# Kernel optimization log

Measured on AMD Instinct MI355X. Metric: run time of the kernel, lower is better.

## Reference

```python
import jax, jax.numpy as jnp
import numpy as np

NLT_SIZES = (10, 19, 39, 69, 12)  # agent, action, duplex, triplet, loc
ALPHA, GAMMA, BETA = 0.25, 2.0, 1.0 / 9.0
B, A, G, T = 8, 60000, 20, 5
C = 1 + sum(NLT_SIZES)  # 150


def setup_inputs() -> dict:
    key = jax.random.key(0)
    ks = jax.random.split(key, 8)
    confidence = jax.random.normal(ks[0], (B, A, C), jnp.float32)
    predicted_locations = jax.random.normal(ks[1], (B, A, 4), jnp.float32)
    gt_locations = jax.random.normal(ks[2], (B, A, 4), jnp.float32)
    counts = jax.random.randint(ks[3], (B,), 1, G + 1, dtype=jnp.int32)
    # gt_labels: [B, G, nlts, T] with -1 tail padding per (gt, label-type) row
    labs = []
    for i, nc in enumerate(NLT_SIZES):
        l = jax.random.randint(jax.random.fold_in(ks[4], i), (B, G, T), 0, nc, dtype=jnp.int32)
        nvalid = jax.random.randint(jax.random.fold_in(ks[5], i), (B, G, 1), 1, T + 1, dtype=jnp.int32)
        l = jnp.where(jnp.arange(T, dtype=jnp.int32)[None, None, :] < nvalid, l, -1)
        labs.append(l)
    gt_labels = jnp.stack(labs, axis=2)  # [B, G, 5, T]
    # labels_bin: per-anchor match result: -1 ignore, 0 background, k in [1, counts[b]] matched gt
    pos_idx = jax.random.randint(ks[6], (B, A), 1, G + 1, dtype=jnp.int32)
    pos_idx = jnp.minimum(pos_idx, counts[:, None])
    u = jax.random.uniform(ks[7], (B, A))
    labels_bin = jnp.where(u < 0.90, 0, jnp.where(u < 0.95, -1, pos_idx)).astype(jnp.int32)
    return {
        "confidence": confidence,
        "predicted_locations": predicted_locations,
        "gt_locations": gt_locations,
        "gt_labels": gt_labels,
        "counts": counts,
        "labels_bin": labels_bin,
    }


def _head_labels(gt_labels_nlt, labels_bin, numc):
    # gt_labels_nlt: [B, G, T] int, -1 tail-padded. Vectorized one_hot_labels + gather.
    valid = (gt_labels_nlt >= 0)
    oh = jax.nn.one_hot(jnp.where(valid, gt_labels_nlt, 0), numc, dtype=jnp.float32)
    oh = oh * valid[..., None].astype(jnp.float32)
    table = (oh.sum(axis=2) > 0).astype(jnp.float32)  # [B, G, numc], multi-hot per gt
    table = jnp.pad(table, ((0, 0), (1, 0), (0, 0)))  # row 0 = background zeros -> [B, G+1, numc]
    idx = jnp.clip(labels_bin, 0, None)  # dumy_conf: ignores (-1) map to row 0
    return jnp.take_along_axis(table, idx[:, :, None], axis=1)  # [B, A, numc]


def _focal(preds, labels, mask, num_pos):
    p = jnp.clip(preds, 1e-7, 1.0 - 1e-7)
    bce = -(labels * jnp.log(p) + (1.0 - labels) * jnp.log1p(-p))
    alpha_factor = ALPHA * labels + (1.0 - ALPHA) * (1.0 - labels)
    pt = p * labels + (1.0 - p) * (1.0 - labels)
    return (bce * alpha_factor * (1.0 - pt) ** GAMMA * mask).sum() / num_pos


def reference(confidence, predicted_locations, gt_locations, gt_labels, counts, labels_bin):
    sig = jax.nn.sigmoid(confidence)
    binary_preds = sig[:, :, 0]
    heads = []
    cc = 1
    for nc in NLT_SIZES:
        heads.append(sig[:, :, cc:cc + nc])
        cc += nc

    pos = (labels_bin > 0).astype(jnp.float32)  # pos_mask
    num_pos = jnp.maximum(1.0, pos.sum())

    n = jnp.abs(predicted_locations - gt_locations)
    sl1 = jnp.where(n < BETA, 0.5 * n * n / BETA, n - 0.5 * BETA)
    regression_loss = (sl1 * pos[:, :, None]).sum() / (num_pos * 4.0)

    mask = (labels_bin > -1).astype(jnp.float32)  # exclude ignored anchors
    cls_loss = 0.0
    for i, nc in enumerate(NLT_SIZES):
        labs = _head_labels(gt_labels[:, :, i, :], labels_bin, nc)
        cls_loss = cls_loss + _focal(heads[i], labs, mask[:, :, None], num_pos)
    cls_loss = cls_loss + _focal(binary_preds, pos, mask, num_pos)  # binary head: labels_bin>0 -> 1
    return (regression_loss, cls_loss / 6.0)
```

## Files before the change

### kernel.cpp

```cpp
#include <hip/hip_runtime.h>

#define B_    8
#define A_    60000
#define C_    150
#define G_    20
#define T_    5
#define ROWS  21
#define NANCH (B_ * A_)
#define NTOT  (B_ * A_ * C_)
#define TABN  (B_ * ROWS * C_)
#define BETA_ (1.0f / 9.0f)

__global__ void build_table(const int* __restrict__ gt_labels,
                            float* __restrict__ tab,
                            float* __restrict__ accum) {
    int i = blockIdx.x * blockDim.x + threadIdx.x;
    if (i < 4) accum[i] = 0.0f;
    if (i >= TABN) return;
    int c  = i % C_;
    int bg = i / C_;
    int g  = bg % ROWS;
    int b  = bg / ROWS;
    float v = 0.0f;
    if (g > 0) {
        if (c == 0) {
            v = 1.0f;
        } else {
            int cc = c - 1;
            int head, k;
            if      (cc < 10)  { head = 0; k = cc; }
            else if (cc < 29)  { head = 1; k = cc - 10; }
            else if (cc < 68)  { head = 2; k = cc - 29; }
            else if (cc < 137) { head = 3; k = cc - 68; }
            else               { head = 4; k = cc - 137; }
            const int* lp = gt_labels + ((b * G_ + (g - 1)) * 5 + head) * T_;
            v = (lp[0] == k || lp[1] == k || lp[2] == k ||
                 lp[3] == k || lp[4] == k) ? 1.0f : 0.0f;
        }
    }
    tab[i] = v;
}

__device__ __forceinline__ float block_reduce_sum(float v, float* sm) {
    #pragma unroll
    for (int off = 32; off > 0; off >>= 1) v += __shfl_down(v, off, 64);
    int lane = threadIdx.x & 63, w = threadIdx.x >> 6;
    if (lane == 0) sm[w] = v;
    __syncthreads();
    float r = 0.0f;
    if (threadIdx.x == 0) r = sm[0] + sm[1] + sm[2] + sm[3];
    __syncthreads();
    return r;
}

__device__ __forceinline__ float sl1(float n) {
    return (n < BETA_) ? (0.5f / BETA_) * n * n : n - 0.5f * BETA_;
}

__global__ __launch_bounds__(256) void reg_kernel(
        const float* __restrict__ pred, const float* __restrict__ gt,
        const int* __restrict__ lb, float* __restrict__ accum) {
    __shared__ float sm[4];
    float reg = 0.0f, cnt = 0.0f;
    int stride = gridDim.x * blockDim.x;
    for (int a = blockIdx.x * blockDim.x + threadIdx.x; a < NANCH; a += stride) {
        int l = lb[a];
        if (l > 0) {
            cnt += 1.0f;
            float4 p = ((const float4*)pred)[a];
            float4 g = ((const float4*)gt)[a];
            reg += sl1(fabsf(p.x - g.x)) + sl1(fabsf(p.y - g.y)) +
                   sl1(fabsf(p.z - g.z)) + sl1(fabsf(p.w - g.w));
        }
    }
    float rblk = block_reduce_sum(reg, sm);
    float cblk = block_reduce_sum(cnt, sm);
    if (threadIdx.x == 0) {
        atomicAdd(&accum[0], rblk);
        atomicAdd(&accum[2], cblk);
    }
}

__global__ __launch_bounds__(256) void cls_kernel(
        const float* __restrict__ conf, const int* __restrict__ lb,
        const float* __restrict__ tab, float* __restrict__ accum) {
    __shared__ float sm[4];
    float acc = 0.0f;
    const float4* cp = (const float4*)conf;
    const int nchunks = NTOT / 4;
    int stride = gridDim.x * blockDim.x;
    for (int ch = blockIdx.x * blockDim.x + threadIdx.x; ch < nchunks; ch += stride) {
        int e = ch * 4;
        float4 x = cp[ch];
        int a  = e / C_;
        int c  = e - a * C_;
        int l0 = lb[a];
        bool spans = (c + 3 >= C_);
        int l1 = spans ? lb[a + 1] : l0;

        if ((l0 | l1) == 0) {
            float xs[4] = {x.x, x.y, x.z, x.w};
            #pragma unroll
            for (int j = 0; j < 4; ++j) {
                float t = __expf(xs[j]);
                float denom = 1.0f + t;
                float om = t * __builtin_amdgcn_rcpf(denom);
                acc += 0.75f * (om * om) * __logf(denom);
            }
        } else if (l0 == -1 && l1 == -1) {
        } else {
            int b0 = a / A_;
            int row0 = (b0 * ROWS + max(l0, 0)) * C_;
            float m0 = (l0 > -1) ? 1.0f : 0.0f;
            int row1 = row0; float m1 = m0;
            if (spans) {
                int b1 = (a + 1) / A_;
                row1 = (b1 * ROWS + max(l1, 0)) * C_;
                m1 = (l1 > -1) ? 1.0f : 0.0f;
            }
            float xs[4] = {x.x, x.y, x.z, x.w};
            #pragma unroll
            for (int j = 0; j < 4; ++j) {
                int cj = c + j;
                int rb; float mf;
                if (cj < C_) { rb = row0 + cj;      mf = m0; }
                else         { rb = row1 + cj - C_; mf = m1; }
                float L = tab[rb];
                float s = (L + L - 1.0f) * xs[j];
                float t = __expf(-s);
                float denom = 1.0f + t;
                float om  = t * __builtin_amdgcn_rcpf(denom);
                float ld  = __logf(denom);
                acc += mf * fmaf(L, -0.5f, 0.75f) * (om * om) * ld;
            }
        }
    }
    float blk = block_reduce_sum(acc, sm);
    if (threadIdx.x == 0) atomicAdd(&accum[1], blk);
}

__global__ void finalize(const float* __restrict__ accum, float* __restrict__ out) {
    float np = fmaxf(1.0f, accum[2]);
    out[0] = accum[0] / (np * 4.0f);
    out[1] = accum[1] / (np * 6.0f);
}

extern "C" void kernel_launch(void* const* d_in, const int* in_sizes, int n_in,
                              void* d_out, int out_size, void* d_ws, size_t ws_size,
                              hipStream_t stream) {
    const float* conf = (const float*)d_in[0];
    const float* pred = (const float*)d_in[1];
    const float* gt   = (const float*)d_in[2];
    const int*   gtl  = (const int*)d_in[3];
    const int*   lb   = (const int*)d_in[5];
    float* out   = (float*)d_out;
    float* accum = (float*)d_ws;
    float* tab   = (float*)d_ws + 64;

    build_table<<<(TABN + 255) / 256, 256, 0, stream>>>(gtl, tab, accum);
    reg_kernel<<<512, 256, 0, stream>>>(pred, gt, lb, accum);
    cls_kernel<<<4096, 256, 0, stream>>>(conf, lb, tab, accum);
    finalize<<<1, 1, 0, stream>>>(accum, out);
}
```

Before: 442.3 us.

## Fuse regression and classification kernels, unroll loads, use deterministic partial reduction

Merges the regression and classification passes into one grid-stride kernel over 8192 blocks. The classification loop is unrolled two-wide so two float4 loads are in flight per thread. The fast background path now uses a wave-uniform __any test, which avoids divergence. Atomics are replaced by per-block partials that a 256-thread finalize kernel reduces. Fully ignored chunks no longer get an early exit and are computed with a zero mask, which adds some transcendental work.

```diff
diff --git a/kernel.cpp b/kernel.cpp
--- a/kernel.cpp
+++ b/kernel.cpp
@@ -1,21 +1,22 @@
 #include <hip/hip_runtime.h>
 
-#define B_    8
-#define A_    60000
-#define C_    150
-#define G_    20
-#define T_    5
-#define ROWS  21
-#define NANCH (B_ * A_)
-#define NTOT  (B_ * A_ * C_)
-#define TABN  (B_ * ROWS * C_)
-#define BETA_ (1.0f / 9.0f)
+#define B_     8
+#define A_     60000
+#define C_     150
+#define G_     20
+#define T_     5
+#define ROWS   21
+#define NANCH  (B_ * A_)
+#define NTOT   (B_ * A_ * C_)
+#define NCHUNK (NTOT / 4)
+#define TABN   (B_ * ROWS * C_)
+#define BETA_  (1.0f / 9.0f)
+#define NBLK   8192
+#define TPB    256
 
 __global__ void build_table(const int* __restrict__ gt_labels,
-                            float* __restrict__ tab,
-                            float* __restrict__ accum) {
+                            float* __restrict__ tab) {
     int i = blockIdx.x * blockDim.x + threadIdx.x;
-    if (i < 4) accum[i] = 0.0f;
     if (i >= TABN) return;
     int c  = i % C_;
     int bg = i / C_;
@@ -57,92 +58,120 @@
     return (n < BETA_) ? (0.5f / BETA_) * n * n : n - 0.5f * BETA_;
 }
 
-__global__ __launch_bounds__(256) void reg_kernel(
-        const float* __restrict__ pred, const float* __restrict__ gt,
-        const int* __restrict__ lb, float* __restrict__ accum) {
+__device__ __forceinline__ float focal_term(float x, float L, float mf) {
+    float s     = (L + L - 1.0f) * x;
+    float t     = __expf(-s);
+    float denom = 1.0f + t;
+    float om    = t * __builtin_amdgcn_rcpf(denom);
+    float ld    = __logf(denom);
+    return mf * fmaf(L, -0.5f, 0.75f) * (om * om) * ld;
+}
+
+__device__ __forceinline__ float process_chunk(float4 x, int a, int c,
+                                               int l0, int l1,
+                                               const float* __restrict__ tab) {
+    float acc = 0.0f;
+    float xs[4] = {x.x, x.y, x.z, x.w};
+    if (!__any((l0 | l1) != 0)) {
+        #pragma unroll
+        for (int j = 0; j < 4; ++j) {
+            float t     = __expf(xs[j]);
+            float denom = 1.0f + t;
+            float om    = t * __builtin_amdgcn_rcpf(denom);
+            acc += 0.75f * (om * om) * __logf(denom);
+        }
+    } else {
+        int   b0   = a / A_;
+        int   row0 = (b0 * ROWS + max(l0, 0)) * C_;
+        float m0   = (l0 > -1) ? 1.0f : 0.0f;
+        int   row1 = row0;
+        float m1   = m0;
+        if (c + 3 >= C_) {
+            int b1 = (a + 1) / A_;
+            row1 = (b1 * ROWS + max(l1, 0)) * C_;
+            m1   = (l1 > -1) ? 1.0f : 0.0f;
+        }
+        #pragma unroll
+        for (int j = 0; j < 4; ++j) {
+            int cj = c + j;
+            int rb; float mf;
+            if (cj < C_) { rb = row0 + cj;       mf = m0; }
+            else         { rb = row1 + cj - C_;  mf = m1; }
+            acc += focal_term(xs[j], tab[rb], mf);
+        }
+    }
+    return acc;
+}
+
+__global__ __launch_bounds__(TPB) void fused_kernel(
+        const float* __restrict__ conf,
+        const float* __restrict__ pred, const float* __restrict__ gtl,
+        const int*   __restrict__ lb,   const float* __restrict__ tab,
+        float* __restrict__ partials) {
     __shared__ float sm[4];
-    float reg = 0.0f, cnt = 0.0f;
-    int stride = gridDim.x * blockDim.x;
-    for (int a = blockIdx.x * blockDim.x + threadIdx.x; a < NANCH; a += stride) {
+    float reg = 0.0f, cls = 0.0f, cnt = 0.0f;
+    const int tid    = blockIdx.x * blockDim.x + threadIdx.x;
+    const int stride = gridDim.x * blockDim.x;
+
+    for (int a = tid; a < NANCH; a += stride) {
         int l = lb[a];
         if (l > 0) {
             cnt += 1.0f;
             float4 p = ((const float4*)pred)[a];
-            float4 g = ((const float4*)gt)[a];
+            float4 g = ((const float4*)gtl)[a];
             reg += sl1(fabsf(p.x - g.x)) + sl1(fabsf(p.y - g.y)) +
                    sl1(fabsf(p.z - g.z)) + sl1(fabsf(p.w - g.w));
         }
     }
-    float rblk = block_reduce_sum(reg, sm);
-    float cblk = block_reduce_sum(cnt, sm);
+
+    const float4* cp = (const float4*)conf;
+    int ch = tid;
+    for (; ch + stride < NCHUNK; ch += 2 * stride) {
+        const int chA = ch, chB = ch + stride;
+        float4 xA = cp[chA];
+        float4 xB = cp[chB];
+        int eA = chA * 4, aA = eA / C_, cA = eA - aA * C_;
+        int eB = chB * 4, aB = eB / C_, cB = eB - aB * C_;
+        int lA0 = lb[aA];
+        int lA1 = (cA + 3 >= C_) ? lb[aA + 1] : lA0;
+        int lB0 = lb[aB];
+        int lB1 = (cB + 3 >= C_) ? lb[aB + 1] : lB0;
+        cls += process_chunk(xA, aA, cA, lA0, lA1, tab);
+        cls += process_chunk(xB, aB, cB, lB0, lB1, tab);
+    }
+    if (ch < NCHUNK) {
+        float4 x = cp[ch];
+        int e = ch * 4, a = e / C_, c = e - a * C_;
+        int l0 = lb[a];
+        int l1 = (c + 3 >= C_) ? lb[a + 1] : l0;
+        cls += process_chunk(x, a, c, l0, l1, tab);
+    }
+
+    float rb = block_reduce_sum(reg, sm);
+    float cb = block_reduce_sum(cls, sm);
+    float nb = block_reduce_sum(cnt, sm);
     if (threadIdx.x == 0) {
-        atomicAdd(&accum[0], rblk);
-        atomicAdd(&accum[2], cblk);
+        float4 w; w.x = rb; w.y = cb; w.z = nb; w.w = 0.0f;
+        ((float4*)partials)[blockIdx.x] = w;
     }
 }
 
-__global__ __launch_bounds__(256) void cls_kernel(
-        const float* __restrict__ conf, const int* __restrict__ lb,
-        const float* __restrict__ tab, float* __restrict__ accum) {
+__global__ __launch_bounds__(TPB) void finalize(
+        const float* __restrict__ partials, float* __restrict__ out) {
     __shared__ float sm[4];
-    float acc = 0.0f;
-    const float4* cp = (const float4*)conf;
-    const int nchunks = NTOT / 4;
-    int stride = gridDim.x * blockDim.x;
-    for (int ch = blockIdx.x * blockDim.x + threadIdx.x; ch < nchunks; ch += stride) {
-        int e = ch * 4;
-        float4 x = cp[ch];
-        int a  = e / C_;
-        int c  = e - a * C_;
-        int l0 = lb[a];
-        bool spans = (c + 3 >= C_);
-        int l1 = spans ? lb[a + 1] : l0;
-
-        if ((l0 | l1) == 0) {
-            float xs[4] = {x.x, x.y, x.z, x.w};
-            #pragma unroll
-            for (int j = 0; j < 4; ++j) {
-                float t = __expf(xs[j]);
-                float denom = 1.0f + t;
-                float om = t * __builtin_amdgcn_rcpf(denom);
-                acc += 0.75f * (om * om) * __logf(denom);
-            }
-        } else if (l0 == -1 && l1 == -1) {
-        } else {
-            int b0 = a / A_;
-            int row0 = (b0 * ROWS + max(l0, 0)) * C_;
-            float m0 = (l0 > -1) ? 1.0f : 0.0f;
-            int row1 = row0; float m1 = m0;
-            if (spans) {
-                int b1 = (a + 1) / A_;
-                row1 = (b1 * ROWS + max(l1, 0)) * C_;
-                m1 = (l1 > -1) ? 1.0f : 0.0f;
-            }
-            float xs[4] = {x.x, x.y, x.z, x.w};
-            #pragma unroll
-            for (int j = 0; j < 4; ++j) {
-                int cj = c + j;
-                int rb; float mf;
-                if (cj < C_) { rb = row0 + cj;      mf = m0; }
-                else         { rb = row1 + cj - C_; mf = m1; }
-                float L = tab[rb];
-                float s = (L + L - 1.0f) * xs[j];
-                float t = __expf(-s);
-                float denom = 1.0f + t;
-                float om  = t * __builtin_amdgcn_rcpf(denom);
-                float ld  = __logf(denom);
-                acc += mf * fmaf(L, -0.5f, 0.75f) * (om * om) * ld;
-            }
-        }
+    float r = 0.0f, c = 0.0f, n = 0.0f;
+    for (int i = threadIdx.x; i < NBLK; i += TPB) {
+        float4 p = ((const float4*)partials)[i];
+        r += p.x; c += p.y; n += p.z;
     }
-    float blk = block_reduce_sum(acc, sm);
-    if (threadIdx.x == 0) atomicAdd(&accum[1], blk);
-}
-
-__global__ void finalize(const float* __restrict__ accum, float* __restrict__ out) {
-    float np = fmaxf(1.0f, accum[2]);
-    out[0] = accum[0] / (np * 4.0f);
-    out[1] = accum[1] / (np * 6.0f);
+    r = block_reduce_sum(r, sm);
+    c = block_reduce_sum(c, sm);
+    n = block_reduce_sum(n, sm);
+    if (threadIdx.x == 0) {
+        float np = fmaxf(1.0f, n);
+        out[0] = r / (np * 4.0f);
+        out[1] = c / (np * 6.0f);
+    }
 }
 
 extern "C" void kernel_launch(void* const* d_in, const int* in_sizes, int n_in,
@@ -153,12 +182,11 @@
     const float* gt   = (const float*)d_in[2];
     const int*   gtl  = (const int*)d_in[3];
     const int*   lb   = (const int*)d_in[5];
-    float* out   = (float*)d_out;
-    float* accum = (float*)d_ws;
-    float* tab   = (float*)d_ws + 64;
+    float* out      = (float*)d_out;
+    float* partials = (float*)d_ws;
+    float* tab      = (float*)d_ws + 4 * NBLK;
 
-    build_table<<<(TABN + 255) / 256, 256, 0, stream>>>(gtl, tab, accum);
-    reg_kernel<<<512, 256, 0, stream>>>(pred, gt, lb, accum);
-    cls_kernel<<<4096, 256, 0, stream>>>(conf, lb, tab, accum);
-    finalize<<<1, 1, 0, stream>>>(accum, out);
+    build_table<<<(TABN + TPB - 1) / TPB, TPB, 0, stream>>>(gtl, tab);
+    fused_kernel<<<NBLK, TPB, 0, stream>>>(conf, pred, gt, lb, tab, partials);
+    finalize<<<1, TPB, 0, stream>>>(partials, out);
 }
```

Measured after the change: 408.6 us. 1.08x faster.
